# Optimization experiments

Hardware: AMD Instinct MI355X
Metric: run time of the kernel (lower is better)

The kernel has to match this reference:

```python
import jax, jax.numpy as jnp
import numpy as np

N = 1_000_000
MU_PRIOR = 0.6447


def setup_inputs() -> dict:
    key = jax.random.key(0)
    ks = jax.random.split(key, 8)
    pred_ = jax.random.normal(ks[0], (N, 9), jnp.float32)
    Y_obs = jax.random.normal(ks[1], (N, 9), jnp.float32)
    rrs = jax.random.normal(ks[2], (N, 5), jnp.float32)
    rrs_pred = jax.random.normal(ks[3], (N, 5), jnp.float32)
    nan_array = jax.random.normal(ks[4], (N, 9), jnp.float32)  # all finite -> lens = 9
    # cov_z must be SPD so log(det(cov_z)) is finite
    A = jax.random.normal(ks[5], (N, 3, 3), jnp.float32) * 0.3
    cov_z = jnp.einsum('nij,nkj->nik', A, A) + 0.5 * jnp.eye(3, dtype=jnp.float32)
    mu_z = jax.random.normal(ks[6], (N, 3), jnp.float32)
    parameters = 1.0 + 0.01 * jax.random.normal(ks[7], (64,), jnp.float32)
    return {"pred_": pred_, "Y_obs": Y_obs, "rrs": rrs, "rrs_pred": rrs_pred,
            "nan_array": nan_array, "cov_z": cov_z, "mu_z": mu_z,
            "parameters": parameters}


def reference(pred_, Y_obs, rrs, rrs_pred, nan_array, cov_z, mu_z, parameters):
    n = pred_.shape[0]
    # --- buffers built in __init__ (default multipliers = ones) ---
    se_diag = jnp.asarray([0.0015, 0.0012, 0.001, 0.00086, 0.00057], jnp.float32) ** 2
    rrs_cov_inv = jnp.linalg.inv(jnp.diag(se_diag))            # [5,5]
    Y_cov_inv = jnp.eye(9, dtype=jnp.float32)                  # [9,9]
    s_a = jnp.eye(3, dtype=jnp.float32) * 4.9                  # [3,3]
    s_a_inv = jnp.linalg.inv(s_a)                              # [3,3]

    # trace((X) @ Cinv @ X.T) == sum_n x_n^T Cinv x_n  (trace trick, O(N))
    dr = rrs - rrs_pred                                        # [N,5]
    rrs_error = jnp.einsum('ni,ij,nj->', dr, rrs_cov_inv, dr) / (5.0 * n)

    lens = jnp.sum(~jnp.isnan(nan_array), axis=1).astype(jnp.float32)  # [N]
    dy = pred_ - Y_obs                                         # [N,9]
    obs_quad = jnp.einsum('ni,ij,nj->n', dy, Y_cov_inv, dy)    # [N]
    obs_error = jnp.sum(obs_quad / lens) / n

    # KL(N(mu_z, cov_z) || N(0.6447, s_a)) style term
    logdet_sa = jnp.log(jnp.linalg.det(s_a))
    logdet_cz = jnp.log(jnp.linalg.det(cov_z))                 # [N]
    tr_term = jnp.einsum('ij,nji->n', s_a_inv, cov_z)          # trace(s_a_inv @ cov_z)
    dm = mu_z - MU_PRIOR                                       # [N,3]
    DK = 0.5 * jnp.sum(logdet_sa - logdet_cz + tr_term) / n \
         + 0.5 * jnp.einsum('ni,ij,nj->', dm, s_a_inv, dm) / (3.0 * n)

    l2_norm = jnp.mean((parameters - 1.0) ** 2)
    return rrs_error + 10.0 * obs_error + DK + l2_norm
```

## Files before the change

### kernel.cpp

```cpp
#include <hip/hip_runtime.h>
#include <math.h>

#define MU_PRIOR   0.6447f
#define LOGDET_SA  4.767705615349743f
#define INV_SA     (1.0f/4.9f)

#define GRID    1024

#define W0 (1.0f / (0.0015f  * 0.0015f))
#define W1 (1.0f / (0.0012f  * 0.0012f))
#define W2 (1.0f / (0.0010f  * 0.0010f))
#define W3 (1.0f / (0.00086f * 0.00086f))
#define W4 (1.0f / (0.00057f * 0.00057f))

typedef float f4_t __attribute__((ext_vector_type(4)));
typedef f4_t uf4 __attribute__((aligned(4)));
typedef float f2_t __attribute__((ext_vector_type(2)));
typedef f2_t uf2 __attribute__((aligned(4)));

__device__ __forceinline__ float warp_reduce_f(float v) {
#pragma unroll
    for (int off = 32; off > 0; off >>= 1) v += __shfl_down(v, off, 64);
    return v;
}

__device__ __forceinline__ double warp_reduce_d(double v) {
#pragma unroll
    for (int off = 32; off > 0; off >>= 1) v += __shfl_down(v, off, 64);
    return v;
}

__global__ __launch_bounds__(256) void loss_main(
    const float* __restrict__ pred, const float* __restrict__ yobs,
    const float* __restrict__ rrs,  const float* __restrict__ rrsp,
    const float* __restrict__ nanarr, const float* __restrict__ cov,
    const float* __restrict__ mu, double* __restrict__ partial, int rows)
{
    const int tid    = blockIdx.x * 256 + threadIdx.x;
    const int stride = (int)gridDim.x * 256;

    float acc = 0.0f;

#pragma unroll 2
    for (int r = tid; r < rows; r += stride) {
        const float* P = pred   + 9 * (size_t)r;
        const float* Y = yobs   + 9 * (size_t)r;
        const float* A = nanarr + 9 * (size_t)r;
        const float* C = cov    + 9 * (size_t)r;
        const float* R = rrs    + 5 * (size_t)r;
        const float* Q = rrsp   + 5 * (size_t)r;
        const float* M = mu     + 3 * (size_t)r;

        const uf4 p0 = *(const uf4*)P;       const uf4 p1 = *(const uf4*)(P + 4);
        const float p8 = P[8];
        const uf4 y0 = *(const uf4*)Y;       const uf4 y1 = *(const uf4*)(Y + 4);
        const float y8 = Y[8];
        const uf4 a0 = *(const uf4*)A;       const uf4 a1 = *(const uf4*)(A + 4);
        const float a8 = A[8];
        const uf4 c0 = *(const uf4*)C;       const uf4 c1 = *(const uf4*)(C + 4);
        const float c8 = C[8];
        const uf4 r0 = *(const uf4*)R;       const float r4 = R[4];
        const uf4 q0 = *(const uf4*)Q;       const float q4 = Q[4];
        const uf2 m0 = *(const uf2*)M;       const float m2 = M[2];

        float dy2, len;
        {
            const float d0 = p0.x - y0.x, d1 = p0.y - y0.y;
            const float d2 = p0.z - y0.z, d3 = p0.w - y0.w;
            const float d4 = p1.x - y1.x, d5 = p1.y - y1.y;
            const float d6 = p1.z - y1.z, d7 = p1.w - y1.w;
            const float d8 = p8 - y8;
            dy2 = d0*d0 + d1*d1 + d2*d2 + d3*d3 + d4*d4
                + d5*d5 + d6*d6 + d7*d7 + d8*d8;
            len = ((a0.x == a0.x) ? 1.f : 0.f) + ((a0.y == a0.y) ? 1.f : 0.f)
                + ((a0.z == a0.z) ? 1.f : 0.f) + ((a0.w == a0.w) ? 1.f : 0.f)
                + ((a1.x == a1.x) ? 1.f : 0.f) + ((a1.y == a1.y) ? 1.f : 0.f)
                + ((a1.z == a1.z) ? 1.f : 0.f) + ((a1.w == a1.w) ? 1.f : 0.f)
                + ((a8   == a8  ) ? 1.f : 0.f);
        }
        acc += 10.0f * dy2 / len;

        {
            const float tr  = c0.x + c1.x + c8;
            const float det = c0.x * (c1.x * c8   - c1.y * c1.w)
                            - c0.y * (c0.w * c8   - c1.y * c1.z)
                            + c0.z * (c0.w * c1.w - c1.x * c1.z);
            acc += 0.5f * (LOGDET_SA - __logf(det) + tr * INV_SA);
        }

        {
            const float d0 = r0.x - q0.x, d1 = r0.y - q0.y;
            const float d2 = r0.z - q0.z, d3 = r0.w - q0.w;
            const float d4 = r4 - q4;
            acc += (d0*d0*W0 + d1*d1*W1 + d2*d2*W2 + d3*d3*W3 + d4*d4*W4)
                   * 0.2f;
        }

        {
            const float d0 = m0.x - MU_PRIOR, d1 = m0.y - MU_PRIOR;
            const float d2 = m2 - MU_PRIOR;
            acc += (d0*d0 + d1*d1 + d2*d2) * (1.0f / 29.4f);
        }
    }

    acc = warp_reduce_f(acc);
    __shared__ float smem[4];
    const int lane = threadIdx.x & 63;
    const int wid  = threadIdx.x >> 6;
    if (lane == 0) smem[wid] = acc;
    __syncthreads();
    if (threadIdx.x == 0)
        partial[blockIdx.x] = (double)(smem[0] + smem[1] + smem[2] + smem[3]);
}

__global__ __launch_bounds__(256) void loss_final(
    const double* __restrict__ partial, int npartials,
    const float* __restrict__ params, int nparams,
    int rows, float* __restrict__ out)
{
    double accA = 0.0;
    double accB = 0.0;

    for (int i = threadIdx.x; i < npartials; i += 256) accA += partial[i];
    for (int i = threadIdx.x; i < nparams; i += 256) {
        const float d = params[i] - 1.0f;
        accB += (double)(d * d);
    }

    double val = accA * (1.0 / (double)rows) + accB * (1.0 / (double)nparams);
    val = warp_reduce_d(val);
    __shared__ double sm[4];
    const int lane = threadIdx.x & 63;
    const int wid  = threadIdx.x >> 6;
    if (lane == 0) sm[wid] = val;
    __syncthreads();
    if (threadIdx.x == 0)
        out[0] = (float)(sm[0] + sm[1] + sm[2] + sm[3]);
}

extern "C" void kernel_launch(void* const* d_in, const int* in_sizes, int n_in,
                              void* d_out, int out_size, void* d_ws, size_t ws_size,
                              hipStream_t stream) {
    const float* pred   = (const float*)d_in[0];
    const float* yobs   = (const float*)d_in[1];
    const float* rrs    = (const float*)d_in[2];
    const float* rrsp   = (const float*)d_in[3];
    const float* nanarr = (const float*)d_in[4];
    const float* cov    = (const float*)d_in[5];
    const float* mu     = (const float*)d_in[6];
    const float* params = (const float*)d_in[7];
    float* out = (float*)d_out;

    const int rows = in_sizes[0] / 9;

    int grid = (rows + 255) / 256;
    if (grid > GRID) grid = GRID;
    if (grid < 1) grid = 1;

    double* partial = (double*)d_ws;

    loss_main<<<grid, 256, 0, stream>>>(pred, yobs, rrs, rrsp, nanarr,
                                        cov, mu, partial, rows);
    loss_final<<<1, 256, 0, stream>>>(partial, grid, params, in_sizes[7],
                                      rows, out);
}
```

Baseline: 206.7 us.

## Split loss kernel into per-term block groups sized by bytes read

Each of the four loss terms now gets its own slice of blocks, sized in proportion to the bytes it reads (108/36/40/12 of 196). The grid doubles to 2048 blocks. The goal is that each thread streams fewer arrays at once, with more blocks in flight to hide memory latency. The cost is that each term's loop runs separately, and each block group streams its arrays with a wider stride.

```diff
diff --git a/kernel.cpp b/kernel.cpp
--- a/kernel.cpp
+++ b/kernel.cpp
@@ -5,7 +5,7 @@
 #define LOGDET_SA  4.767705615349743f
 #define INV_SA     (1.0f/4.9f)
 
-#define GRID    1024
+#define TOTALBLK 2048
 
 #define W0 (1.0f / (0.0015f  * 0.0015f))
 #define W1 (1.0f / (0.0012f  * 0.0012f))
@@ -34,69 +34,79 @@
     const float* __restrict__ pred, const float* __restrict__ yobs,
     const float* __restrict__ rrs,  const float* __restrict__ rrsp,
     const float* __restrict__ nanarr, const float* __restrict__ cov,
-    const float* __restrict__ mu, double* __restrict__ partial, int rows)
+    const float* __restrict__ mu, double* __restrict__ partial, int rows,
+    int aB, int bB, int cB)
 {
-    const int tid    = blockIdx.x * 256 + threadIdx.x;
-    const int stride = (int)gridDim.x * 256;
-
+    const int b = (int)blockIdx.x;
     float acc = 0.0f;
 
+    if (b < aB) {
+        const int t0     = b * 256 + (int)threadIdx.x;
+        const int stride = aB * 256;
 #pragma unroll 2
-    for (int r = tid; r < rows; r += stride) {
-        const float* P = pred   + 9 * (size_t)r;
-        const float* Y = yobs   + 9 * (size_t)r;
-        const float* A = nanarr + 9 * (size_t)r;
-        const float* C = cov    + 9 * (size_t)r;
-        const float* R = rrs    + 5 * (size_t)r;
-        const float* Q = rrsp   + 5 * (size_t)r;
-        const float* M = mu     + 3 * (size_t)r;
+        for (int r = t0; r < rows; r += stride) {
+            const float* P = pred   + 9 * (size_t)r;
+            const float* Y = yobs   + 9 * (size_t)r;
+            const float* A = nanarr + 9 * (size_t)r;
+            const uf4 p0 = *(const uf4*)P; const uf4 p1 = *(const uf4*)(P + 4);
+            const float p8 = P[8];
+            const uf4 y0 = *(const uf4*)Y; const uf4 y1 = *(const uf4*)(Y + 4);
+            const float y8 = Y[8];
+            const uf4 a0 = *(const uf4*)A; const uf4 a1 = *(const uf4*)(A + 4);
+            const float a8 = A[8];
 
-        const uf4 p0 = *(const uf4*)P;       const uf4 p1 = *(const uf4*)(P + 4);
-        const float p8 = P[8];
-        const uf4 y0 = *(const uf4*)Y;       const uf4 y1 = *(const uf4*)(Y + 4);
-        const float y8 = Y[8];
-        const uf4 a0 = *(const uf4*)A;       const uf4 a1 = *(const uf4*)(A + 4);
-        const float a8 = A[8];
-        const uf4 c0 = *(const uf4*)C;       const uf4 c1 = *(const uf4*)(C + 4);
-        const float c8 = C[8];
-        const uf4 r0 = *(const uf4*)R;       const float r4 = R[4];
-        const uf4 q0 = *(const uf4*)Q;       const float q4 = Q[4];
-        const uf2 m0 = *(const uf2*)M;       const float m2 = M[2];
-
-        float dy2, len;
-        {
             const float d0 = p0.x - y0.x, d1 = p0.y - y0.y;
             const float d2 = p0.z - y0.z, d3 = p0.w - y0.w;
             const float d4 = p1.x - y1.x, d5 = p1.y - y1.y;
             const float d6 = p1.z - y1.z, d7 = p1.w - y1.w;
             const float d8 = p8 - y8;
-            dy2 = d0*d0 + d1*d1 + d2*d2 + d3*d3 + d4*d4
-                + d5*d5 + d6*d6 + d7*d7 + d8*d8;
-            len = ((a0.x == a0.x) ? 1.f : 0.f) + ((a0.y == a0.y) ? 1.f : 0.f)
+            const float dy2 = d0*d0 + d1*d1 + d2*d2 + d3*d3 + d4*d4
+                            + d5*d5 + d6*d6 + d7*d7 + d8*d8;
+            const float len =
+                  ((a0.x == a0.x) ? 1.f : 0.f) + ((a0.y == a0.y) ? 1.f : 0.f)
                 + ((a0.z == a0.z) ? 1.f : 0.f) + ((a0.w == a0.w) ? 1.f : 0.f)
                 + ((a1.x == a1.x) ? 1.f : 0.f) + ((a1.y == a1.y) ? 1.f : 0.f)
                 + ((a1.z == a1.z) ? 1.f : 0.f) + ((a1.w == a1.w) ? 1.f : 0.f)
                 + ((a8   == a8  ) ? 1.f : 0.f);
+            acc += 10.0f * dy2 / len;
         }
-        acc += 10.0f * dy2 / len;
-
-        {
+    } else if (b < aB + bB) {
+        const int t0     = (b - aB) * 256 + (int)threadIdx.x;
+        const int stride = bB * 256;
+#pragma unroll 2
+        for (int r = t0; r < rows; r += stride) {
+            const float* C = cov + 9 * (size_t)r;
+            const uf4 c0 = *(const uf4*)C; const uf4 c1 = *(const uf4*)(C + 4);
+            const float c8 = C[8];
             const float tr  = c0.x + c1.x + c8;
             const float det = c0.x * (c1.x * c8   - c1.y * c1.w)
                             - c0.y * (c0.w * c8   - c1.y * c1.z)
                             + c0.z * (c0.w * c1.w - c1.x * c1.z);
             acc += 0.5f * (LOGDET_SA - __logf(det) + tr * INV_SA);
         }
-
-        {
+    } else if (b < aB + bB + cB) {
+        const int t0     = (b - aB - bB) * 256 + (int)threadIdx.x;
+        const int stride = cB * 256;
+#pragma unroll 2
+        for (int r = t0; r < rows; r += stride) {
+            const float* R = rrs  + 5 * (size_t)r;
+            const float* Q = rrsp + 5 * (size_t)r;
+            const uf4 r0 = *(const uf4*)R; const float r4 = R[4];
+            const uf4 q0 = *(const uf4*)Q; const float q4 = Q[4];
             const float d0 = r0.x - q0.x, d1 = r0.y - q0.y;
             const float d2 = r0.z - q0.z, d3 = r0.w - q0.w;
             const float d4 = r4 - q4;
             acc += (d0*d0*W0 + d1*d1*W1 + d2*d2*W2 + d3*d3*W3 + d4*d4*W4)
                    * 0.2f;
         }
-
-        {
+    } else {
+        const int dB     = (int)gridDim.x - aB - bB - cB;
+        const int t0     = (b - aB - bB - cB) * 256 + (int)threadIdx.x;
+        const int stride = dB * 256;
+#pragma unroll 2
+        for (int r = t0; r < rows; r += stride) {
+            const float* M = mu + 3 * (size_t)r;
+            const uf2 m0 = *(const uf2*)M; const float m2 = M[2];
             const float d0 = m0.x - MU_PRIOR, d1 = m0.y - MU_PRIOR;
             const float d2 = m2 - MU_PRIOR;
             acc += (d0*d0 + d1*d1 + d2*d2) * (1.0f / 29.4f);
@@ -153,14 +163,18 @@
 
     const int rows = in_sizes[0] / 9;
 
-    int grid = (rows + 255) / 256;
-    if (grid > GRID) grid = GRID;
-    if (grid < 1) grid = 1;
+    int aB = (TOTALBLK * 108) / 196;
+    int bB = (TOTALBLK *  36) / 196;
+    int cB = (TOTALBLK *  40) / 196;
+    if (aB < 1) aB = 1;
+    if (bB < 1) bB = 1;
+    if (cB < 1) cB = 1;
+    int grid = TOTALBLK;
 
     double* partial = (double*)d_ws;
 
     loss_main<<<grid, 256, 0, stream>>>(pred, yobs, rrs, rrsp, nanarr,
-                                        cov, mu, partial, rows);
+                                        cov, mu, partial, rows, aB, bB, cB);
     loss_final<<<1, 256, 0, stream>>>(partial, grid, params, in_sizes[7],
                                       rows, out);
 }
```

After: 214.9 us. +3.9%, slower.
